# Kernel optimization log

Hardware: AMD Instinct MI355X
Metric: run time of the kernel (lower is better)

## Reference

```python
import jax, jax.numpy as jnp
import numpy as np

NU, NPOI, NC = 500000, 200000, 100
E_UP, E_PP = 500000, 1000000
H = 32


def _lin_params(key, fan_in, fan_out):
    k1, k2 = jax.random.split(key)
    s = 1.0 / np.sqrt(fan_in)
    W = jax.random.uniform(k1, (fan_in, fan_out), minval=-s, maxval=s, dtype=jnp.float32)
    b = jax.random.uniform(k2, (fan_out,), minval=-s, maxval=s, dtype=jnp.float32)
    return W, b


def setup_inputs() -> dict:
    key = jax.random.key(0)
    ks = jax.random.split(key, 40)
    inp = {}
    inp['x_user'] = jax.random.normal(ks[0], (NU, 2), jnp.float32)
    inp['x_poi'] = jax.random.normal(ks[1], (NPOI, 3), jnp.float32)
    inp['x_cate'] = jax.random.normal(ks[2], (NC, 1), jnp.float32)
    names = ['user_lin', 'poi_lin', 'cate_lin', 'W1_u', 'W1_p', 'W1_c', 'W1_pp', 'W2_u', 'W2_p', 'W2_c', 'W2_pp']
    fan_ins = [2, 3, 1, H, H, H, H, H, H, H, H]
    for i, (n, fi) in enumerate(zip(names, fan_ins)):
        W, b = _lin_params(ks[3 + i], fi, H)
        inp[n + '_w'] = W
        inp[n + '_b'] = b
    inp['cate_emb'] = jax.random.normal(ks[20], (100, H), jnp.float32)

    def edges(k, n_src, n_dst, e):
        k1, k2 = jax.random.split(k)
        return jnp.stack([jax.random.randint(k1, (e,), 0, n_src),
                          jax.random.randint(k2, (e,), 0, n_dst)]).astype(jnp.int32)

    inp['ei_pv'] = edges(ks[21], NU, NPOI, E_UP)
    inp['ei_mc'] = edges(ks[22], NU, NPOI, E_UP)
    inp['ei_order'] = edges(ks[23], NU, NPOI, E_UP)
    inp['ei_rev_pv'] = edges(ks[24], NPOI, NU, E_UP)
    inp['ei_rev_mc'] = edges(ks[25], NPOI, NU, E_UP)
    inp['ei_rev_order'] = edges(ks[26], NPOI, NU, E_UP)
    inp['ei_belongs'] = edges(ks[27], NC, NPOI, NPOI)
    inp['ei_pp'] = edges(ks[28], NPOI, NPOI, E_PP)
    for i, n in enumerate(['ea_pv', 'ea_mc', 'ea_order', 'ea_rev_pv', 'ea_rev_mc', 'ea_rev_order']):
        inp[n] = jax.random.uniform(ks[29 + i], (E_UP,), jnp.float32)
    inp['ea_pp'] = jax.random.uniform(ks[35], (E_PP,), jnp.float32)
    return inp


def _prop(src_h, ei, W, b, ea, dst_h):
    # gather -> linear -> (edge weight) -> scatter-mean -> relu residual
    msg = src_h[ei[0]] @ W + b  # [E, H]
    if ea is not None:
        msg = msg * ea[:, None]
    n = dst_h.shape[0]
    s = jax.ops.segment_sum(msg, ei[1], num_segments=n)
    c = jax.ops.segment_sum(jnp.ones((ei.shape[1],), msg.dtype), ei[1], num_segments=n)
    # nodes with no incoming edges get agg=0 -> relu(0)=0, matching the torch
    # unique/scatter_add + count-clamp formulation exactly.
    return dst_h + jax.nn.relu(s / jnp.maximum(c, 1.0)[:, None])


def reference(x_user, x_poi, x_cate,
              user_lin_w, user_lin_b, poi_lin_w, poi_lin_b, cate_lin_w, cate_lin_b,
              W1_u_w, W1_u_b, W1_p_w, W1_p_b, W1_c_w, W1_c_b, W1_pp_w, W1_pp_b,
              W2_u_w, W2_u_b, W2_p_w, W2_p_b, W2_c_w, W2_c_b, W2_pp_w, W2_pp_b,
              cate_emb,
              ea_pv, ea_mc, ea_order, ea_rev_pv, ea_rev_mc, ea_rev_order, ea_pp,
              ei_pv, ei_mc, ei_order, ei_rev_pv, ei_rev_mc, ei_rev_order, ei_belongs, ei_pp):
    user_h = jax.nn.relu(x_user @ user_lin_w + user_lin_b)
    poi_h = jax.nn.relu(x_poi @ poi_lin_w + poi_lin_b)
    cate_h = jax.nn.relu(x_cate @ cate_lin_w + cate_lin_b) + cate_emb[:x_cate.shape[0]]
    # --- layer 1 ---
    for ei, ea in [(ei_rev_pv, ea_rev_pv), (ei_rev_mc, ea_rev_mc), (ei_rev_order, ea_rev_order)]:
        user_h = _prop(poi_h, ei, W1_p_w, W1_p_b, ea, user_h)
    for ei, ea in [(ei_pv, ea_pv), (ei_mc, ea_mc), (ei_order, ea_order)]:
        poi_h = _prop(user_h, ei, W1_u_w, W1_u_b, ea, poi_h)
    poi_h = _prop(cate_h, ei_belongs, W1_c_w, W1_c_b, None, poi_h)
    poi_h = _prop(poi_h, ei_pp, W1_pp_w, W1_pp_b, ea_pp, poi_h)
    # dropout is identity in eval mode
    # --- layer 2 ---
    for ei, ea in [(ei_rev_pv, ea_rev_pv), (ei_rev_mc, ea_rev_mc), (ei_rev_order, ea_rev_order)]:
        user_h = _prop(poi_h, ei, W2_p_w, W2_p_b, ea, user_h)
    for ei, ea in [(ei_pv, ea_pv), (ei_mc, ea_mc), (ei_order, ea_order)]:
        poi_h = _prop(user_h, ei, W2_u_w, W2_u_b, ea, poi_h)
    poi_h = _prop(cate_h, ei_belongs, W2_c_w, W2_c_b, None, poi_h)
    poi_h = _prop(poi_h, ei_pp, W2_pp_w, W2_pp_b, ea_pp, poi_h)
    # concatenate the three node-type outputs along node axis: [NU+NPOI+NC, H]
    return jnp.concatenate([user_h, poi_h, cate_h], axis=0)
```

## Files before the change

### kernel.cpp

```cpp
#include <hip/hip_runtime.h>

#define HDIM 32

typedef unsigned int uint32;

static constexpr int NU   = 500000;
static constexpr int NPOI = 200000;
static constexpr int NC   = 100;
static constexpr int E_UP = 500000;
static constexpr int E_PP = 1000000;

static constexpr int NLISTS = 8;
static constexpr int TOT_E  = 6 * E_UP + NPOI + E_PP;
static constexpr int TOT_R4 = 4 * NU + 8 * NPOI;
static constexpr int TOT_R1 = 3 * NU + 5 * NPOI;

static constexpr int BSH  = 12;
static constexpr int BSZ  = 1 << BSH;
static constexpr int NB   = (TOT_R4 + BSZ - 1) / BSZ;
static constexpr int CNTN = 512;
static constexpr int BCH  = 2048;

__global__ void zero_kernel(int* __restrict__ p, int n) {
    int i = blockIdx.x * blockDim.x + threadIdx.x;
    int stride = gridDim.x * blockDim.x;
    for (; i < n; i += stride) p[i] = 0;
}

__global__ void copyi(const int* __restrict__ a, int* __restrict__ b, int n) {
    int i = blockIdx.x * blockDim.x + threadIdx.x;
    if (i < n) b[i] = a[i];
}

__global__ void init_nodes(const float* __restrict__ x, int fin,
                           const float* __restrict__ W, const float* __restrict__ b,
                           const float* __restrict__ emb,
                           float* __restrict__ h, int n) {
    int idx = blockIdx.x * blockDim.x + threadIdx.x;
    if (idx >= n * HDIM) return;
    int i = idx >> 5, f = idx & 31;
    float r = b[f];
    for (int k = 0; k < fin; ++k) r += x[i * fin + k] * W[k * HDIM + f];
    r = fmaxf(r, 0.0f);
    if (emb) r += emb[idx];
    h[idx] = r;
}

struct BL {
    const int* ei[NLISTS];
    const float* ea[NLISTS];
    int E[NLISTS];
    int lbase[NLISTS];
    int lslot[NLISTS];
    int shift[NLISTS];
    int coff[NLISTS];
};

__global__ __launch_bounds__(256) void bin_count(BL P, int* __restrict__ BB) {
    __shared__ int cnt[CNTN];
    int w = blockIdx.x;
    int l = 0;
    while (l < NLISTS - 1 && w >= P.coff[l + 1]) ++l;
    int e0 = (w - P.coff[l]) * BCH;
    int E = P.E[l];
    const int* dstp = P.ei[l] + E;
    int lbase = P.lbase[l], lslot = P.lslot[l];
    int cbase = lbase >> BSH;
    for (int i = threadIdx.x; i < CNTN; i += 256) cnt[i] = 0;
    __syncthreads();
    int e1 = min(e0 + BCH, E);
    for (int e = e0 + threadIdx.x; e < e1; e += 256) {
        int slot = lbase + dstp[e] * 4 + lslot;
        atomicAdd(&cnt[(slot >> BSH) - cbase], 1);
    }
    __syncthreads();
    for (int i = threadIdx.x; i < CNTN; i += 256) {
        int c = cnt[i];
        if (c > 0) atomicAdd(&BB[cbase + i], c);
    }
}

__global__ __launch_bounds__(256) void bin_place(BL P, int* __restrict__ Gcur,
                                                 int2* __restrict__ S2,
                                                 int* __restrict__ D) {
    __shared__ int cnt[CNTN];
    __shared__ int cur[CNTN];
    int w = blockIdx.x;
    int l = 0;
    while (l < NLISTS - 1 && w >= P.coff[l + 1]) ++l;
    int e0 = (w - P.coff[l]) * BCH;
    int E = P.E[l];
    const int* srcp = P.ei[l];
    const int* dstp = P.ei[l] + E;
    const float* eap = P.ea[l];
    int lbase = P.lbase[l], lslot = P.lslot[l], shift = P.shift[l];
    int cbase = lbase >> BSH;
    for (int i = threadIdx.x; i < CNTN; i += 256) cnt[i] = 0;
    __syncthreads();
    int e1 = min(e0 + BCH, E);

    int slot_[8], my_[8], sw_[8], wb_[8];
    bool ok_[8];
#pragma unroll
    for (int k = 0; k < 8; ++k) {
        int e = e0 + k * 256 + threadIdx.x;
        ok_[k] = (e < e1);
        if (ok_[k]) {
            slot_[k] = lbase + dstp[e] * 4 + lslot;
            sw_[k] = srcp[e] << shift;
            wb_[k] = eap ? __float_as_int(eap[e]) : __float_as_int(1.0f);
            my_[k] = atomicAdd(&cnt[(slot_[k] >> BSH) - cbase], 1);
        }
    }
    __syncthreads();
    for (int i = threadIdx.x; i < CNTN; i += 256) {
        int c = cnt[i];
        cur[i] = (c > 0) ? atomicAdd(&Gcur[cbase + i], c) : 0;
    }
    __syncthreads();
#pragma unroll
    for (int k = 0; k < 8; ++k) {
        if (ok_[k]) {
            int g = cur[(slot_[k] >> BSH) - cbase] + my_[k];
            S2[g] = make_int2(sw_[k], wb_[k]);
            D[g] = slot_[k];
        }
    }
}

__global__ __launch_bounds__(256) void csr_place(const int* __restrict__ BB,
                                                 const int2* __restrict__ S2,
                                                 const int* __restrict__ D,
                                                 int* __restrict__ R,
                                                 int2* __restrict__ esw) {
    __shared__ int cnt[BSZ];
    __shared__ int wpart[256];
    int b = blockIdx.x;
    int s0 = b << BSH;
    int ns = min(BSZ, TOT_R4 - s0);
    int j0 = BB[b], j1 = BB[b + 1];
    for (int i = threadIdx.x; i < BSZ; i += 256) cnt[i] = 0;
    __syncthreads();
    for (int j = j0 + threadIdx.x; j < j1; j += 256)
        atomicAdd(&cnt[D[j] - s0], 1);
    __syncthreads();
    int v[16]; int s = 0;
    int base = threadIdx.x * 16;
#pragma unroll
    for (int k = 0; k < 16; ++k) { v[k] = cnt[base + k]; s += v[k]; }
    wpart[threadIdx.x] = s;
    __syncthreads();
    for (int off = 1; off < 256; off <<= 1) {
        int t = (threadIdx.x >= off) ? wpart[threadIdx.x - off] : 0;
        __syncthreads(); wpart[threadIdx.x] += t; __syncthreads();
    }
    int run = wpart[threadIdx.x] - s;
#pragma unroll
    for (int k = 0; k < 16; ++k) { cnt[base + k] = run; run += v[k]; }
    __syncthreads();
    for (int i = threadIdx.x; i < ns; i += 256) R[s0 + i] = j0 + cnt[i];
    __syncthreads();
    for (int j = j0 + threadIdx.x; j < j1; j += 256) {
        int sl = D[j];
        int p = j0 + atomicAdd(&cnt[sl - s0], 1);
        esw[p] = S2[j];
    }
}

__global__ void hist1(const int* __restrict__ ei_dst, int E, int* __restrict__ R,
                      int base, int stride, int slot) {
    int e = blockIdx.x * blockDim.x + threadIdx.x;
    if (e < E) atomicAdd(&R[base + ei_dst[e] * stride + slot], 1);
}

#define SCAN_T 256
#define SCAN_ELEMS 4
#define SCAN_CHUNK (SCAN_T * SCAN_ELEMS)

__global__ void scan1(int* __restrict__ R, int N, int* __restrict__ part) {
    __shared__ int lds[SCAN_T];
    int base = blockIdx.x * SCAN_CHUNK + threadIdx.x * SCAN_ELEMS;
    int v[SCAN_ELEMS]; int s = 0;
#pragma unroll
    for (int k = 0; k < SCAN_ELEMS; ++k) { int i = base + k; v[k] = (i < N) ? R[i] : 0; s += v[k]; }
    lds[threadIdx.x] = s; __syncthreads();
    for (int off = 1; off < SCAN_T; off <<= 1) {
        int t = (threadIdx.x >= off) ? lds[threadIdx.x - off] : 0;
        __syncthreads(); lds[threadIdx.x] += t; __syncthreads();
    }
    int incl = lds[threadIdx.x];
    int total = lds[SCAN_T - 1];
    int run = incl - s;
#pragma unroll
    for (int k = 0; k < SCAN_ELEMS; ++k) { int i = base + k; if (i < N) R[i] = run; run += v[k]; }
    if (threadIdx.x == 0) part[blockIdx.x] = total;
}

__global__ void scan2(int* __restrict__ part, int nb) {
    __shared__ int lds[SCAN_T];
    __shared__ int carry;
    if (threadIdx.x == 0) carry = 0;
    __syncthreads();
    for (int base = 0; base < nb; base += SCAN_T) {
        int i = base + threadIdx.x;
        int v = (i < nb) ? part[i] : 0;
        lds[threadIdx.x] = v; __syncthreads();
        for (int off = 1; off < SCAN_T; off <<= 1) {
            int t = (threadIdx.x >= off) ? lds[threadIdx.x - off] : 0;
            __syncthreads(); lds[threadIdx.x] += t; __syncthreads();
        }
        int incl = lds[threadIdx.x]; int tot = lds[SCAN_T - 1];
        if (i < nb) part[i] = carry + incl - v;
        __syncthreads();
        if (threadIdx.x == 0) carry += tot;
        __syncthreads();
    }
}

__global__ void scan3(int* __restrict__ R, int N, const int* __restrict__ part) {
    int base = blockIdx.x * SCAN_CHUNK + threadIdx.x * SCAN_ELEMS;
    int add = part[blockIdx.x];
#pragma unroll
    for (int k = 0; k < SCAN_ELEMS; ++k) { int i = base + k; if (i < N) R[i] += add; }
}

__global__ void fill1(const int* __restrict__ ei, const float* __restrict__ ea,
                      int E, int* __restrict__ R, int base, int stride, int slot,
                      int shift, int2* __restrict__ esw) {
    int e = blockIdx.x * blockDim.x + threadIdx.x;
    if (e >= E) return;
    int d = ei[E + e];
    int pos = atomicAdd(&R[base + d * stride + slot], 1);
    float w = ea ? ea[e] : 1.0f;
    esw[pos] = make_int2(ei[e] << shift, __float_as_int(w));
}

__device__ inline unsigned short bf16rn(float f) {
    uint32 u = __float_as_uint(f);
    return (unsigned short)((u + 0x7fffu + ((u >> 16) & 1u)) >> 16);
}

__global__ __launch_bounds__(256) void transform_k(const float* __restrict__ src,
                                                   const float* __restrict__ W,
                                                   const float* __restrict__ b,
                                                   float* __restrict__ out, int n) {
    int idx = blockIdx.x * blockDim.x + threadIdx.x;
    if (idx >= n * HDIM) return;
    int f = idx & 31;
    float Wc[HDIM];
#pragma unroll
    for (int k = 0; k < HDIM; ++k) Wc[k] = W[k * HDIM + f];
    float x = src[idx];
    float r = b[f];
#pragma unroll
    for (int k = 0; k < HDIM; ++k) r += __shfl(x, k, 32) * Wc[k];
    out[idx] = r;
}

__global__ __launch_bounds__(256) void transform_bf16_k(const float* __restrict__ src,
                                                        const float* __restrict__ W,
                                                        const float* __restrict__ b,
                                                        unsigned short* __restrict__ out,
                                                        int n) {
    int idx = blockIdx.x * blockDim.x + threadIdx.x;
    if (idx >= n * HDIM) return;
    int f = idx & 31;
    float Wc[HDIM];
#pragma unroll
    for (int k = 0; k < HDIM; ++k) Wc[k] = W[k * HDIM + f];
    float x = src[idx];
    float r = b[f];
#pragma unroll
    for (int k = 0; k < HDIM; ++k) r += __shfl(x, k, 32) * Wc[k];
    out[idx] = bf16rn(r);
}

__global__ void copy4(const float4* __restrict__ src, float4* __restrict__ dst, int n4) {
    int i = blockIdx.x * blockDim.x + threadIdx.x;
    int stride = gridDim.x * blockDim.x;
    for (; i < n4; i += stride) dst[i] = src[i];
}

__device__ inline float4 ldrow_f32(const char* base, uint32 off, int lane8) {
    return ((const float4*)(base + off))[lane8];
}
__device__ inline float4 ldrow_bf16(const char* base, uint32 off, int lane8) {
    uint2 q = ((const uint2*)(base + off))[lane8];
    float4 v;
    v.x = __uint_as_float(q.x << 16);
    v.y = __uint_as_float(q.x & 0xffff0000u);
    v.z = __uint_as_float(q.y << 16);
    v.w = __uint_as_float(q.y & 0xffff0000u);
    return v;
}

template<int NSEG, bool SRCBF16, bool HASB, bool EPI, bool EPIBF16>
__global__ __launch_bounds__(256) void prop_k(
    float4* __restrict__ dst4,
    const char* __restrict__ srcB,
    const char* __restrict__ srcB2,
    const int4* __restrict__ R4,
    const int2* __restrict__ esw,
    const float4* __restrict__ WT4, const float4* __restrict__ bT4,
    void* __restrict__ dstT, int n)
{
    __shared__ float4 Ws4[HDIM][8];
    __shared__ float4 bTs[8];
    if (EPI) {
        int t = threadIdx.x;
        { int k = t >> 3, j = t & 7; Ws4[k][j] = WT4[k * 8 + j]; }
        if (t < 8) bTs[t] = bT4[t];
        __syncthreads();
    }
    int grp = threadIdx.x >> 3, lane8 = threadIdx.x & 7;
    int r = blockIdx.x * 32 + grp;
    if (r >= n) return;

    int4 ev = R4[r];
    int s0 = ev.x;
    int zend = (NSEG == 3) ? ev.w : ev.y;

    float4 acc = make_float4(0.f, 0.f, 0.f, 0.f);
    float4 res = make_float4(0.f, 0.f, 0.f, 0.f);
    int segs = s0;

    if (s0 < zend) {
        int last = zend - 1;
        int2 eA = esw[s0];
        int2 eB = esw[min(s0 + 1, last)];
        float4 vA = SRCBF16 ? ldrow_bf16(srcB, (uint32)eA.x, lane8)
                            : ldrow_f32 (srcB, (uint32)eA.x, lane8);
        for (int j = s0; j < zend; ++j) {
            float4 vB = SRCBF16 ? ldrow_bf16(srcB, (uint32)eB.x, lane8)
                                : ldrow_f32 (srcB, (uint32)eB.x, lane8);
            int2 eC = esw[min(j + 2, last)];
            float w = __int_as_float(eA.y);
            acc.x += w * vA.x; acc.y += w * vA.y;
            acc.z += w * vA.z; acc.w += w * vA.w;
            int j1 = j + 1;
            bool fin = (j1 == ev.y) || (NSEG == 3 && ((j1 == ev.z) | (j1 == ev.w)));
            if (fin) {
                float inv = __builtin_amdgcn_rcpf((float)(j1 - segs));
                res.x += fmaxf(acc.x * inv, 0.f);
                res.y += fmaxf(acc.y * inv, 0.f);
                res.z += fmaxf(acc.z * inv, 0.f);
                res.w += fmaxf(acc.w * inv, 0.f);
                acc = make_float4(0.f, 0.f, 0.f, 0.f);
                segs = j1;
            }
            eA = eB; eB = eC; vA = vB;
        }
    }
    int ctot = zend - s0;
    if (HASB) {
        int nx = R4[r + 1].x;
        int c2 = nx - ev.w;
        float4 a2 = make_float4(0.f, 0.f, 0.f, 0.f);
        for (int j = ev.w; j < nx; ++j) {
            int2 e = esw[j];
            float w = __int_as_float(e.y);
            float4 v = ldrow_f32(srcB2, (uint32)e.x, lane8);
            a2.x += w * v.x; a2.y += w * v.y; a2.z += w * v.z; a2.w += w * v.w;
        }
        if (c2 > 0) {
            float inv = __builtin_amdgcn_rcpf((float)c2);
            res.x += fmaxf(a2.x * inv, 0.f);
            res.y += fmaxf(a2.y * inv, 0.f);
            res.z += fmaxf(a2.z * inv, 0.f);
            res.w += fmaxf(a2.w * inv, 0.f);
        }
        ctot += c2;
    }

    float4* dp = dst4 + (size_t)r * 8 + lane8;
    float4 dv = *dp;
    if (ctot) {
        dv.x += res.x; dv.y += res.y; dv.z += res.z; dv.w += res.w;
        *dp = dv;
    }

    if (EPI) {
        float4 to = bTs[lane8];
#pragma unroll
        for (int sl = 0; sl < 8; ++sl) {
            float ux = __shfl(dv.x, sl, 8);
            float uy = __shfl(dv.y, sl, 8);
            float uz = __shfl(dv.z, sl, 8);
            float uw = __shfl(dv.w, sl, 8);
            float4 w0 = Ws4[sl * 4 + 0][lane8];
            to.x += ux * w0.x; to.y += ux * w0.y; to.z += ux * w0.z; to.w += ux * w0.w;
            float4 w1 = Ws4[sl * 4 + 1][lane8];
            to.x += uy * w1.x; to.y += uy * w1.y; to.z += uy * w1.z; to.w += uy * w1.w;
            float4 w2 = Ws4[sl * 4 + 2][lane8];
            to.x += uz * w2.x; to.y += uz * w2.y; to.z += uz * w2.z; to.w += uz * w2.w;
            float4 w3 = Ws4[sl * 4 + 3][lane8];
            to.x += uw * w3.x; to.y += uw * w3.y; to.z += uw * w3.z; to.w += uw * w3.w;
        }
        if (EPIBF16) {
            ushort4 h;
            h.x = bf16rn(to.x); h.y = bf16rn(to.y);
            h.z = bf16rn(to.z); h.w = bf16rn(to.w);
            ((ushort4*)dstT)[(size_t)r * 8 + lane8] = h;
        } else {
            ((float4*)dstT)[(size_t)r * 8 + lane8] = to;
        }
    }
}

template<int NL>
__global__ __launch_bounds__(256) void row_prop_fb(
    float* __restrict__ dst, const char* __restrict__ srcB,
    const int* __restrict__ R, const int2* __restrict__ esw,
    int ro0, int ro1, int ro2, int eo0, int eo1, int eo2,
    const float* __restrict__ W, const float* __restrict__ b, int n) {
    __shared__ float Ws[HDIM * HDIM];
    for (int i = threadIdx.x; i < HDIM * HDIM; i += blockDim.x) Ws[i] = W[i];
    __syncthreads();
    int r = blockIdx.x * (blockDim.x >> 5) + (threadIdx.x >> 5);
    if (r >= n) return;
    int f = threadIdx.x & 31;
    float bf = b[f];
    float res = 0.0f;
    int ctot = 0;
#pragma unroll
    for (int l = 0; l < NL; ++l) {
        int ro = (l == 0) ? ro0 : (l == 1) ? ro1 : ro2;
        int eo = (l == 0) ? eo0 : (l == 1) ? eo1 : eo2;
        int jcur = (r == 0) ? eo : R[ro + r - 1];
        int jend = R[ro + r];
        int c = jend - jcur;
        float acc = 0.0f, t = 0.0f;
        for (int j = jcur; j < jend; ++j) {
            int2 e = esw[j];
            float w = __int_as_float(e.y);
            acc += w * ((const float*)(srcB + (size_t)(uint32)e.x))[f];
            t += w;
        }
        ctot += c;
        float rl = t * bf;
#pragma unroll
        for (int k = 0; k < HDIM; ++k) rl += __shfl(acc, k, 32) * Ws[k * HDIM + f];
        rl /= fmaxf((float)c, 1.0f);
        res += fmaxf(rl, 0.0f);
    }
    if (ctot > 0) dst[(size_t)r * HDIM + f] += res;
}

extern "C" void kernel_launch(void* const* d_in, const int* in_sizes, int n_in,
                              void* d_out, int out_size, void* d_ws, size_t ws_size,
                              hipStream_t stream) {
    const float* x_user = (const float*)d_in[0];
    const float* x_poi  = (const float*)d_in[1];
    const float* x_cate = (const float*)d_in[2];
    const float* ulw    = (const float*)d_in[3];
    const float* ulb    = (const float*)d_in[4];
    const float* plw    = (const float*)d_in[5];
    const float* plb    = (const float*)d_in[6];
    const float* clw    = (const float*)d_in[7];
    const float* clb    = (const float*)d_in[8];
    const float* W1u_w  = (const float*)d_in[9];   const float* W1u_b  = (const float*)d_in[10];
    const float* W1p_w  = (const float*)d_in[11];  const float* W1p_b  = (const float*)d_in[12];
    const float* W1c_w  = (const float*)d_in[13];  const float* W1c_b  = (const float*)d_in[14];
    const float* W1pp_w = (const float*)d_in[15];  const float* W1pp_b = (const float*)d_in[16];
    const float* W2u_w  = (const float*)d_in[17];  const float* W2u_b  = (const float*)d_in[18];
    const float* W2p_w  = (const float*)d_in[19];  const float* W2p_b  = (const float*)d_in[20];
    const float* W2c_w  = (const float*)d_in[21];  const float* W2c_b  = (const float*)d_in[22];
    const float* W2pp_w = (const float*)d_in[23];  const float* W2pp_b = (const float*)d_in[24];
    const float* cate_emb = (const float*)d_in[25];
    const int* ei_pv        = (const int*)d_in[26];
    const int* ei_mc        = (const int*)d_in[27];
    const int* ei_order     = (const int*)d_in[28];
    const int* ei_rev_pv    = (const int*)d_in[29];
    const int* ei_rev_mc    = (const int*)d_in[30];
    const int* ei_rev_order = (const int*)d_in[31];
    const int* ei_belongs   = (const int*)d_in[32];
    const int* ei_pp        = (const int*)d_in[33];
    const float* ea_pv        = (const float*)d_in[34];
    const float* ea_mc        = (const float*)d_in[35];
    const float* ea_order     = (const float*)d_in[36];
    const float* ea_rev_pv    = (const float*)d_in[37];
    const float* ea_rev_mc    = (const float*)d_in[38];
    const float* ea_rev_order = (const float*)d_in[39];
    const float* ea_pp        = (const float*)d_in[40];

    float* user_h = (float*)d_out;
    float* poi_h  = user_h + (size_t)NU * HDIM;
    float* cate_h = poi_h + (size_t)NPOI * HDIM;

    const int* eis[NLISTS] = {ei_rev_pv, ei_rev_mc, ei_rev_order,
                              ei_pv, ei_mc, ei_order, ei_belongs, ei_pp};
    const float* eas[NLISTS] = {ea_rev_pv, ea_rev_mc, ea_rev_order,
                                ea_pv, ea_mc, ea_order, nullptr, ea_pp};
    const int Es[NLISTS] = {E_UP, E_UP, E_UP, E_UP, E_UP, E_UP, NPOI, E_PP};

    dim3 blk(256);

    size_t szR  = (size_t)(TOT_R4 + 4) * 4;
    size_t szE  = (size_t)TOT_E * 8;
    size_t szBG = 16384;
    size_t szT  = (size_t)NU * 64 + 2 * (size_t)NPOI * 64;
    size_t szC  = (size_t)NC * HDIM * 4;
    size_t need_new = szR + szE + szBG + szT + szC + 256;
    bool pret = (ws_size >= need_new);

    if (pret) {
        int*  R    = (int*)d_ws;
        int2* esw  = (int2*)(R + TOT_R4 + 4);
        int*  BB   = (int*)(esw + TOT_E);
        int*  Gcur = BB + (NB + 1);
        char* Tbase = (char*)(((size_t)(Gcur + NB) + 255) & ~(size_t)255);
        unsigned short* userT = (unsigned short*)Tbase;
        unsigned short* poiTA = userT + (size_t)NU * HDIM;
        unsigned short* poiTB = poiTA + (size_t)NPOI * HDIM;
        int2* S2 = (int2*)Tbase;
        int*  D  = (int*)(S2 + TOT_E);
        float* cateT = (float*)(Tbase + szT);

        const int BU = 0, BF = 4 * NU, BP = 4 * NU + 4 * NPOI;
        BL P;
        const int Lbase[NLISTS]  = {BU, BU, BU, BF, BF, BF, BF, BP};
        const int Lslot[NLISTS]  = {0, 1, 2, 0, 1, 2, 3, 0};
        const int Lshift[NLISTS] = {6, 6, 6, 6, 6, 6, 7, 6};
        int co = 0;
        for (int l = 0; l < NLISTS; ++l) {
            P.ei[l] = eis[l]; P.ea[l] = eas[l]; P.E[l] = Es[l];
            P.lbase[l] = Lbase[l]; P.lslot[l] = Lslot[l]; P.shift[l] = Lshift[l];
            P.coff[l] = co;
            co += (Es[l] + BCH - 1) / BCH;
        }
        int nwg = co;

        hipLaunchKernelGGL(zero_kernel, dim3(8), blk, 0, stream, BB, 2 * NB + 1);
        hipLaunchKernelGGL(bin_count, dim3(nwg), blk, 0, stream, P, BB);
        hipLaunchKernelGGL(scan2, dim3(1), dim3(SCAN_T), 0, stream, BB, NB + 1);
        hipLaunchKernelGGL(copyi, dim3((NB + 255) / 256), blk, 0, stream, BB, Gcur, NB);
        hipLaunchKernelGGL(bin_place, dim3(nwg), blk, 0, stream, P, Gcur, S2, D);
        hipLaunchKernelGGL(csr_place, dim3(NB), blk, 0, stream, BB, S2, D, R, esw);

        hipLaunchKernelGGL(init_nodes, dim3((NU * HDIM + 255) / 256), blk, 0, stream,
                           x_user, 2, ulw, ulb, (const float*)nullptr, user_h, NU);
        hipLaunchKernelGGL(init_nodes, dim3((NPOI * HDIM + 255) / 256), blk, 0, stream,
                           x_poi, 3, plw, plb, (const float*)nullptr, poi_h, NPOI);
        hipLaunchKernelGGL(init_nodes, dim3((NC * HDIM + 255) / 256), blk, 0, stream,
                           x_cate, 1, clw, clb, cate_emb, cate_h, NC);

        dim3 g_u((NU + 31) / 32), g_p((NPOI + 31) / 32);
        dim3 gtp((NPOI * HDIM + 255) / 256), gtc((NC * HDIM + 255) / 256);

        hipLaunchKernelGGL(transform_bf16_k, gtp, blk, 0, stream, poi_h, W1p_w, W1p_b, poiTA, NPOI);
        hipLaunchKernelGGL(transform_k, gtc, blk, 0, stream, cate_h, W1c_w, W1c_b, cateT, NC);

        hipLaunchKernelGGL((prop_k<3, true, false, true, true>), g_u, blk, 0, stream,
                           (float4*)user_h, (const char*)poiTA, (const char*)nullptr,
                           (const int4*)(R + BU), esw,
                           (const float4*)W1u_w, (const float4*)W1u_b, (void*)userT, NU);
        hipLaunchKernelGGL((prop_k<3, true, true, true, true>), g_p, blk, 0, stream,
                           (float4*)poi_h, (const char*)userT, (const char*)cateT,
                           (const int4*)(R + BF), esw,
                           (const float4*)W1pp_w, (const float4*)W1pp_b, (void*)poiTB, NPOI);
        hipLaunchKernelGGL((prop_k<1, true, false, true, true>), g_p, blk, 0, stream,
                           (float4*)poi_h, (const char*)poiTB, (const char*)nullptr,
                           (const int4*)(R + BP), esw,
                           (const float4*)W2p_w, (const float4*)W2p_b, (void*)poiTA, NPOI);

        hipLaunchKernelGGL(transform_k, gtc, blk, 0, stream, cate_h, W2c_w, W2c_b, cateT, NC);
        hipLaunchKernelGGL((prop_k<3, true, false, true, true>), g_u, blk, 0, stream,
                           (float4*)user_h, (const char*)poiTA, (const char*)nullptr,
                           (const int4*)(R + BU), esw,
                           (const float4*)W2u_w, (const float4*)W2u_b, (void*)userT, NU);
        hipLaunchKernelGGL((prop_k<3, true, true, true, true>), g_p, blk, 0, stream,
                           (float4*)poi_h, (const char*)userT, (const char*)cateT,
                           (const int4*)(R + BF), esw,
                           (const float4*)W2pp_w, (const float4*)W2pp_b, (void*)poiTB, NPOI);
        hipLaunchKernelGGL((prop_k<1, true, false, false, false>), g_p, blk, 0, stream,
                           (float4*)poi_h, (const char*)poiTB, (const char*)nullptr,
                           (const int4*)(R + BP), esw,
                           (const float4*)nullptr, (const float4*)nullptr, (void*)nullptr, NPOI);
    } else {
        int*   R    = (int*)d_ws;
        int2*  esw  = (int2*)(R + TOT_R1);
        int*   part = (int*)(esw + TOT_E);
        float* snap = (float*)(part + 4096);

        const int ns[NLISTS] = {NU, NU, NU, NPOI, NPOI, NPOI, NPOI, NPOI};
        int eoff[NLISTS], roff[NLISTS];
        { int eo = 0, ro = 0;
          for (int l = 0; l < NLISTS; ++l) { eoff[l] = eo; roff[l] = ro; eo += Es[l]; ro += ns[l]; } }

        hipLaunchKernelGGL(zero_kernel, dim3(2048), blk, 0, stream, R, TOT_R1);
        for (int l = 0; l < NLISTS; ++l)
            hipLaunchKernelGGL(hist1, dim3((Es[l] + 255) / 256), blk, 0, stream,
                               eis[l] + Es[l], Es[l], R, roff[l], 1, 0);
        int nb = (TOT_R1 + SCAN_CHUNK - 1) / SCAN_CHUNK;
        hipLaunchKernelGGL(scan1, dim3(nb), dim3(SCAN_T), 0, stream, R, TOT_R1, part);
        hipLaunchKernelGGL(scan2, dim3(1), dim3(SCAN_T), 0, stream, part, nb);
        hipLaunchKernelGGL(scan3, dim3(nb), dim3(SCAN_T), 0, stream, R, TOT_R1, part);
        for (int l = 0; l < NLISTS; ++l)
            hipLaunchKernelGGL(fill1, dim3((Es[l] + 255) / 256), blk, 0, stream,
                               eis[l], eas[l], Es[l], R, roff[l], 1, 0, 7, esw);

        hipLaunchKernelGGL(init_nodes, dim3((NU * HDIM + 255) / 256), blk, 0, stream,
                           x_user, 2, ulw, ulb, (const float*)nullptr, user_h, NU);
        hipLaunchKernelGGL(init_nodes, dim3((NPOI * HDIM + 255) / 256), blk, 0, stream,
                           x_poi, 3, plw, plb, (const float*)nullptr, poi_h, NPOI);
        hipLaunchKernelGGL(init_nodes, dim3((NC * HDIM + 255) / 256), blk, 0, stream,
                           x_cate, 1, clw, clb, cate_emb, cate_h, NC);

        dim3 gu((NU + 7) / 8), gp((NPOI + 7) / 8);
        int n4 = NPOI * HDIM / 4;

        for (int layer = 0; layer < 2; ++layer) {
            const float* Wp  = layer ? W2p_w  : W1p_w;   const float* bp  = layer ? W2p_b  : W1p_b;
            const float* Wu  = layer ? W2u_w  : W1u_w;   const float* bu  = layer ? W2u_b  : W1u_b;
            const float* Wc  = layer ? W2c_w  : W1c_w;   const float* bc  = layer ? W2c_b  : W1c_b;
            const float* Wpp = layer ? W2pp_w : W1pp_w;  const float* bpp = layer ? W2pp_b : W1pp_b;

            hipLaunchKernelGGL((row_prop_fb<3>), gu, blk, 0, stream,
                               user_h, (const char*)poi_h, R, esw,
                               roff[0], roff[1], roff[2], eoff[0], eoff[1], eoff[2],
                               Wp, bp, NU);
            hipLaunchKernelGGL((row_prop_fb<3>), gp, blk, 0, stream,
                               poi_h, (const char*)user_h, R, esw,
                               roff[3], roff[4], roff[5], eoff[3], eoff[4], eoff[5],
                               Wu, bu, NPOI);
            hipLaunchKernelGGL((row_prop_fb<1>), gp, blk, 0, stream,
                               poi_h, (const char*)cate_h, R, esw,
                               roff[6], 0, 0, eoff[6], 0, 0, Wc, bc, NPOI);
            hipLaunchKernelGGL(copy4, dim3(4096), blk, 0, stream,
                               (const float4*)poi_h, (float4*)snap, n4);
            hipLaunchKernelGGL((row_prop_fb<1>), gp, blk, 0, stream,
                               poi_h, (const char*)snap, R, esw,
                               roff[7], 0, 0, eoff[7], 0, 0, Wpp, bpp, NPOI);
        }
    }
}
```

Baseline: 599.1 us.

## Fuse node init into transform and prop kernels, pack slot into binned records

Drops the separate user/poi init_nodes launches. The poi input linear+relu is now recomputed inside the first bf16 transform, and the user/poi initial features are computed in the epilogue of the first-layer prop kernels instead of being read from memory. The binning pass packs the local slot into the low bits of the source index, so the separate D array is no longer written or read, and the per-list shift is applied later in csr_place. This cuts several full-size global reads and writes in the graph-build and init stages, at the cost of extra template parameters and some recomputed arithmetic.

```diff
diff --git a/kernel.cpp b/kernel.cpp
--- a/kernel.cpp
+++ b/kernel.cpp
@@ -20,6 +20,10 @@
 static constexpr int NB   = (TOT_R4 + BSZ - 1) / BSZ;
 static constexpr int CNTN = 512;
 static constexpr int BCH  = 2048;
+
+static constexpr int BU_ = 0;
+static constexpr int BF_ = 4 * NU;
+static constexpr int BP_ = 4 * NU + 4 * NPOI;
 
 __global__ void zero_kernel(int* __restrict__ p, int n) {
     int i = blockIdx.x * blockDim.x + threadIdx.x;
@@ -52,7 +56,6 @@
     int E[NLISTS];
     int lbase[NLISTS];
     int lslot[NLISTS];
-    int shift[NLISTS];
     int coff[NLISTS];
 };
 
@@ -81,8 +84,7 @@
 }
 
 __global__ __launch_bounds__(256) void bin_place(BL P, int* __restrict__ Gcur,
-                                                 int2* __restrict__ S2,
-                                                 int* __restrict__ D) {
+                                                 int2* __restrict__ S2) {
     __shared__ int cnt[CNTN];
     __shared__ int cur[CNTN];
     int w = blockIdx.x;
@@ -93,23 +95,24 @@
     const int* srcp = P.ei[l];
     const int* dstp = P.ei[l] + E;
     const float* eap = P.ea[l];
-    int lbase = P.lbase[l], lslot = P.lslot[l], shift = P.shift[l];
+    int lbase = P.lbase[l], lslot = P.lslot[l];
     int cbase = lbase >> BSH;
     for (int i = threadIdx.x; i < CNTN; i += 256) cnt[i] = 0;
     __syncthreads();
     int e1 = min(e0 + BCH, E);
 
-    int slot_[8], my_[8], sw_[8], wb_[8];
+    int pk_[8], my_[8], wb_[8], li_[8];
     bool ok_[8];
 #pragma unroll
     for (int k = 0; k < 8; ++k) {
         int e = e0 + k * 256 + threadIdx.x;
         ok_[k] = (e < e1);
         if (ok_[k]) {
-            slot_[k] = lbase + dstp[e] * 4 + lslot;
-            sw_[k] = srcp[e] << shift;
+            int slot = lbase + dstp[e] * 4 + lslot;
+            li_[k] = (slot >> BSH) - cbase;
+            pk_[k] = (srcp[e] << BSH) | (slot & (BSZ - 1));
             wb_[k] = eap ? __float_as_int(eap[e]) : __float_as_int(1.0f);
-            my_[k] = atomicAdd(&cnt[(slot_[k] >> BSH) - cbase], 1);
+            my_[k] = atomicAdd(&cnt[li_[k]], 1);
         }
     }
     __syncthreads();
@@ -121,16 +124,14 @@
 #pragma unroll
     for (int k = 0; k < 8; ++k) {
         if (ok_[k]) {
-            int g = cur[(slot_[k] >> BSH) - cbase] + my_[k];
-            S2[g] = make_int2(sw_[k], wb_[k]);
-            D[g] = slot_[k];
+            int g = cur[li_[k]] + my_[k];
+            S2[g] = make_int2(pk_[k], wb_[k]);
         }
     }
 }
 
 __global__ __launch_bounds__(256) void csr_place(const int* __restrict__ BB,
                                                  const int2* __restrict__ S2,
-                                                 const int* __restrict__ D,
                                                  int* __restrict__ R,
                                                  int2* __restrict__ esw) {
     __shared__ int cnt[BSZ];
@@ -142,7 +143,7 @@
     for (int i = threadIdx.x; i < BSZ; i += 256) cnt[i] = 0;
     __syncthreads();
     for (int j = j0 + threadIdx.x; j < j1; j += 256)
-        atomicAdd(&cnt[D[j] - s0], 1);
+        atomicAdd(&cnt[S2[j].x & (BSZ - 1)], 1);
     __syncthreads();
     int v[16]; int s = 0;
     int base = threadIdx.x * 16;
@@ -161,9 +162,13 @@
     for (int i = threadIdx.x; i < ns; i += 256) R[s0 + i] = j0 + cnt[i];
     __syncthreads();
     for (int j = j0 + threadIdx.x; j < j1; j += 256) {
-        int sl = D[j];
-        int p = j0 + atomicAdd(&cnt[sl - s0], 1);
-        esw[p] = S2[j];
+        int2 rec = S2[j];
+        int ls = rec.x & (BSZ - 1);
+        uint32 src = (uint32)rec.x >> BSH;
+        int slot = s0 + ls;
+        int shift = (slot >= BF_ && slot < BP_ && (slot & 3) == 3) ? 7 : 6;
+        int p = j0 + atomicAdd(&cnt[ls], 1);
+        esw[p] = make_int2((int)(src << shift), rec.y);
     }
 }
 
@@ -257,21 +262,23 @@
     out[idx] = r;
 }
 
-__global__ __launch_bounds__(256) void transform_bf16_k(const float* __restrict__ src,
-                                                        const float* __restrict__ W,
-                                                        const float* __restrict__ b,
-                                                        unsigned short* __restrict__ out,
-                                                        int n) {
+__global__ __launch_bounds__(256) void transform_init_bf16(
+    const float* __restrict__ x, int fin,
+    const float* __restrict__ Wi, const float* __restrict__ bi,
+    const float* __restrict__ W, const float* __restrict__ b,
+    unsigned short* __restrict__ out, int n) {
     int idx = blockIdx.x * blockDim.x + threadIdx.x;
     if (idx >= n * HDIM) return;
-    int f = idx & 31;
+    int i = idx >> 5, f = idx & 31;
+    float h = bi[f];
+    for (int k = 0; k < fin; ++k) h += x[i * fin + k] * Wi[k * HDIM + f];
+    h = fmaxf(h, 0.0f);
     float Wc[HDIM];
 #pragma unroll
     for (int k = 0; k < HDIM; ++k) Wc[k] = W[k * HDIM + f];
-    float x = src[idx];
     float r = b[f];
 #pragma unroll
-    for (int k = 0; k < HDIM; ++k) r += __shfl(x, k, 32) * Wc[k];
+    for (int k = 0; k < HDIM; ++k) r += __shfl(h, k, 32) * Wc[k];
     out[idx] = bf16rn(r);
 }
 
@@ -294,7 +301,7 @@
     return v;
 }
 
-template<int NSEG, bool SRCBF16, bool HASB, bool EPI, bool EPIBF16>
+template<int NSEG, bool SRCBF16, bool HASB, bool EPI, bool EPIBF16, int FIN>
 __global__ __launch_bounds__(256) void prop_k(
     float4* __restrict__ dst4,
     const char* __restrict__ srcB,
@@ -302,16 +309,25 @@
     const int4* __restrict__ R4,
     const int2* __restrict__ esw,
     const float4* __restrict__ WT4, const float4* __restrict__ bT4,
-    void* __restrict__ dstT, int n)
+    void* __restrict__ dstT,
+    const float* __restrict__ xin, const float* __restrict__ Wi,
+    const float* __restrict__ bi, int n)
 {
     __shared__ float4 Ws4[HDIM][8];
     __shared__ float4 bTs[8];
+    __shared__ float Wis[3 * HDIM];
+    __shared__ float bis[HDIM];
     if (EPI) {
         int t = threadIdx.x;
         { int k = t >> 3, j = t & 7; Ws4[k][j] = WT4[k * 8 + j]; }
         if (t < 8) bTs[t] = bT4[t];
-        __syncthreads();
-    }
+    }
+    if (FIN > 0) {
+        if (threadIdx.x < FIN * HDIM) Wis[threadIdx.x] = Wi[threadIdx.x];
+        if (threadIdx.x < HDIM) bis[threadIdx.x] = bi[threadIdx.x];
+    }
+    if (EPI || FIN > 0) __syncthreads();
+
     int grp = threadIdx.x >> 3, lane8 = threadIdx.x & 7;
     int r = blockIdx.x * 32 + grp;
     if (r >= n) return;
@@ -373,11 +389,29 @@
     }
 
     float4* dp = dst4 + (size_t)r * 8 + lane8;
-    float4 dv = *dp;
+    float4 dv;
+    if (FIN > 0) {
+        float xr[FIN > 0 ? FIN : 1];
+#pragma unroll
+        for (int k = 0; k < FIN; ++k) xr[k] = xin[(size_t)r * FIN + k];
+        int f0 = lane8 * 4;
+        dv.x = bis[f0]; dv.y = bis[f0 + 1]; dv.z = bis[f0 + 2]; dv.w = bis[f0 + 3];
+#pragma unroll
+        for (int k = 0; k < FIN; ++k) {
+            dv.x += xr[k] * Wis[k * HDIM + f0];
+            dv.y += xr[k] * Wis[k * HDIM + f0 + 1];
+            dv.z += xr[k] * Wis[k * HDIM + f0 + 2];
+            dv.w += xr[k] * Wis[k * HDIM + f0 + 3];
+        }
+        dv.x = fmaxf(dv.x, 0.f); dv.y = fmaxf(dv.y, 0.f);
+        dv.z = fmaxf(dv.z, 0.f); dv.w = fmaxf(dv.w, 0.f);
+    } else {
+        dv = *dp;
+    }
     if (ctot) {
         dv.x += res.x; dv.y += res.y; dv.z += res.z; dv.w += res.w;
-        *dp = dv;
-    }
+    }
+    if (FIN > 0 || ctot) *dp = dv;
 
     if (EPI) {
         float4 to = bTs[lane8];
@@ -513,18 +547,16 @@
         unsigned short* poiTA = userT + (size_t)NU * HDIM;
         unsigned short* poiTB = poiTA + (size_t)NPOI * HDIM;
         int2* S2 = (int2*)Tbase;
-        int*  D  = (int*)(S2 + TOT_E);
         float* cateT = (float*)(Tbase + szT);
 
-        const int BU = 0, BF = 4 * NU, BP = 4 * NU + 4 * NPOI;
+        const int BU = BU_, BF = BF_, BP = BP_;
         BL P;
         const int Lbase[NLISTS]  = {BU, BU, BU, BF, BF, BF, BF, BP};
         const int Lslot[NLISTS]  = {0, 1, 2, 0, 1, 2, 3, 0};
-        const int Lshift[NLISTS] = {6, 6, 6, 6, 6, 6, 7, 6};
         int co = 0;
         for (int l = 0; l < NLISTS; ++l) {
             P.ei[l] = eis[l]; P.ea[l] = eas[l]; P.E[l] = Es[l];
-            P.lbase[l] = Lbase[l]; P.lslot[l] = Lslot[l]; P.shift[l] = Lshift[l];
+            P.lbase[l] = Lbase[l]; P.lslot[l] = Lslot[l];
             P.coff[l] = co;
             co += (Es[l] + BCH - 1) / BCH;
         }
@@ -534,48 +566,55 @@
         hipLaunchKernelGGL(bin_count, dim3(nwg), blk, 0, stream, P, BB);
         hipLaunchKernelGGL(scan2, dim3(1), dim3(SCAN_T), 0, stream, BB, NB + 1);
         hipLaunchKernelGGL(copyi, dim3((NB + 255) / 256), blk, 0, stream, BB, Gcur, NB);
-        hipLaunchKernelGGL(bin_place, dim3(nwg), blk, 0, stream, P, Gcur, S2, D);
-        hipLaunchKernelGGL(csr_place, dim3(NB), blk, 0, stream, BB, S2, D, R, esw);
-
-        hipLaunchKernelGGL(init_nodes, dim3((NU * HDIM + 255) / 256), blk, 0, stream,
-                           x_user, 2, ulw, ulb, (const float*)nullptr, user_h, NU);
-        hipLaunchKernelGGL(init_nodes, dim3((NPOI * HDIM + 255) / 256), blk, 0, stream,
-                           x_poi, 3, plw, plb, (const float*)nullptr, poi_h, NPOI);
+        hipLaunchKernelGGL(bin_place, dim3(nwg), blk, 0, stream, P, Gcur, S2);
+        hipLaunchKernelGGL(csr_place, dim3(NB), blk, 0, stream, BB, S2, R, esw);
+
         hipLaunchKernelGGL(init_nodes, dim3((NC * HDIM + 255) / 256), blk, 0, stream,
                            x_cate, 1, clw, clb, cate_emb, cate_h, NC);
 
         dim3 g_u((NU + 31) / 32), g_p((NPOI + 31) / 32);
         dim3 gtp((NPOI * HDIM + 255) / 256), gtc((NC * HDIM + 255) / 256);
 
-        hipLaunchKernelGGL(transform_bf16_k, gtp, blk, 0, stream, poi_h, W1p_w, W1p_b, poiTA, NPOI);
+        hipLaunchKernelGGL(transform_init_bf16, gtp, blk, 0, stream,
+                           x_poi, 3, plw, plb, W1p_w, W1p_b, poiTA, NPOI);
         hipLaunchKernelGGL(transform_k, gtc, blk, 0, stream, cate_h, W1c_w, W1c_b, cateT, NC);
 
-        hipLaunchKernelGGL((prop_k<3, true, false, true, true>), g_u, blk, 0, stream,
+        hipLaunchKernelGGL((prop_k<3, true, false, true, true, 2>), g_u, blk, 0, stream,
                            (float4*)user_h, (const char*)poiTA, (const char*)nullptr,
                            (const int4*)(R + BU), esw,
-                           (const float4*)W1u_w, (const float4*)W1u_b, (void*)userT, NU);
-        hipLaunchKernelGGL((prop_k<3, true, true, true, true>), g_p, blk, 0, stream,
+                           (const float4*)W1u_w, (const float4*)W1u_b, (void*)userT,
+                           x_user, ulw, ulb, NU);
+        hipLaunchKernelGGL((prop_k<3, true, true, true, true, 3>), g_p, blk, 0, stream,
                            (float4*)poi_h, (const char*)userT, (const char*)cateT,
                            (const int4*)(R + BF), esw,
-                           (const float4*)W1pp_w, (const float4*)W1pp_b, (void*)poiTB, NPOI);
-        hipLaunchKernelGGL((prop_k<1, true, false, true, true>), g_p, blk, 0, stream,
+                           (const float4*)W1pp_w, (const float4*)W1pp_b, (void*)poiTB,
+                           x_poi, plw, plb, NPOI);
+        hipLaunchKernelGGL((prop_k<1, true, false, true, true, 0>), g_p, blk, 0, stream,
                            (float4*)poi_h, (const char*)poiTB, (const char*)nullptr,
                            (const int4*)(R + BP), esw,
-                           (const float4*)W2p_w, (const float4*)W2p_b, (void*)poiTA, NPOI);
+                           (const float4*)W2p_w, (const float4*)W2p_b, (void*)poiTA,
+                           (const float*)nullptr, (const float*)nullptr,
+                           (const float*)nullptr, NPOI);
 
         hipLaunchKernelGGL(transform_k, gtc, blk, 0, stream, cate_h, W2c_w, W2c_b, cateT, NC);
-        hipLaunchKernelGGL((prop_k<3, true, false, true, true>), g_u, blk, 0, stream,
+        hipLaunchKernelGGL((prop_k<3, true, false, true, true, 0>), g_u, blk, 0, stream,
                            (float4*)user_h, (const char*)poiTA, (const char*)nullptr,
                            (const int4*)(R + BU), esw,
-                           (const float4*)W2u_w, (const float4*)W2u_b, (void*)userT, NU);
-        hipLaunchKernelGGL((prop_k<3, true, true, true, true>), g_p, blk, 0, stream,
+                           (const float4*)W2u_w, (const float4*)W2u_b, (void*)userT,
+                           (const float*)nullptr, (const float*)nullptr,
+                           (const float*)nullptr, NU);
+        hipLaunchKernelGGL((prop_k<3, true, true, true, true, 0>), g_p, blk, 0, stream,
                            (float4*)poi_h, (const char*)userT, (const char*)cateT,
                            (const int4*)(R + BF), esw,
-                           (const float4*)W2pp_w, (const float4*)W2pp_b, (void*)poiTB, NPOI);
-        hipLaunchKernelGGL((prop_k<1, true, false, false, false>), g_p, blk, 0, stream,
+                           (const float4*)W2pp_w, (const float4*)W2pp_b, (void*)poiTB,
+                           (const float*)nullptr, (const float*)nullptr,
+                           (const float*)nullptr, NPOI);
+        hipLaunchKernelGGL((prop_k<1, true, false, false, false, 0>), g_p, blk, 0, stream,
                            (float4*)poi_h, (const char*)poiTB, (const char*)nullptr,
                            (const int4*)(R + BP), esw,
-                           (const float4*)nullptr, (const float4*)nullptr, (void*)nullptr, NPOI);
+                           (const float4*)nullptr, (const float4*)nullptr, (void*)nullptr,
+                           (const float*)nullptr, (const float*)nullptr,
+                           (const float*)nullptr, NPOI);
     } else {
         int*   R    = (int*)d_ws;
         int2*  esw  = (int2*)(R + TOT_R1);
```

Result: faster. 512.7 us, median of 2 (-14.4%).
